# Performance work log

Hardware: AMD Instinct MI355X
Metric: run time of the kernel (lower is better)

Reference implementation:

```python
import jax, jax.numpy as jnp
import numpy as np

IN_FEATURES = 3
MAPPING_SIZE = 128
FF_SCALE = 10.0
HIDDEN = 512
HIDDEN_LAYERS = 5
OUT_FEATURES = 3
OMEGA0 = 30.0
TWO_PI = 2.0 * np.pi


def setup_inputs() -> dict:
    key = jax.random.key(0)
    ks = jax.random.split(key, 10)
    B, L = 1, 262144
    coords = jax.random.uniform(ks[0], (B, L, IN_FEATURES), jnp.float32, -1.0, 1.0)
    # Fourier feature projection (random Gaussian buffer, scale=10)
    B_ff = jax.random.normal(ks[1], (IN_FEATURES, MAPPING_SIZE), jnp.float32) * FF_SCALE
    ff_dim = 2 * MAPPING_SIZE  # 256
    # First sine layer: is_first=True -> U(-1/in, 1/in)
    W_first = jax.random.uniform(ks[2], (HIDDEN, ff_dim), jnp.float32, -1.0 / ff_dim, 1.0 / ff_dim)
    b_first = jax.random.uniform(ks[3], (HIDDEN,), jnp.float32, -1.0 / np.sqrt(ff_dim), 1.0 / np.sqrt(ff_dim))
    # Hidden sine layers: U(-sqrt(6/in)/omega0, +)
    wh = np.sqrt(6.0 / HIDDEN) / OMEGA0
    W_hidden = jax.random.uniform(ks[4], (HIDDEN_LAYERS, HIDDEN, HIDDEN), jnp.float32, -wh, wh)
    b_hidden = jax.random.uniform(ks[5], (HIDDEN_LAYERS, HIDDEN), jnp.float32, -1.0 / np.sqrt(HIDDEN), 1.0 / np.sqrt(HIDDEN))
    # Final linear: U(-sqrt(6/hidden)/omega0, +)
    W_out = jax.random.uniform(ks[6], (OUT_FEATURES, HIDDEN), jnp.float32, -wh, wh)
    b_out = jax.random.uniform(ks[7], (OUT_FEATURES,), jnp.float32, -1.0 / np.sqrt(HIDDEN), 1.0 / np.sqrt(HIDDEN))
    return {"coords": coords, "B_ff": B_ff, "W_first": W_first, "b_first": b_first,
            "W_hidden": W_hidden, "b_hidden": b_hidden, "W_out": W_out, "b_out": b_out}


def reference(coords, B_ff, W_first, b_first, W_hidden, b_hidden, W_out, b_out):
    # Fourier feature encoding: [B,L,3] -> [B,L,256]
    proj = TWO_PI * (coords @ B_ff)
    h = jnp.concatenate([jnp.sin(proj), jnp.cos(proj)], axis=-1)
    # First sine layer
    h = jnp.sin(OMEGA0 * (jnp.einsum('bli,oi->blo', h, W_first) + b_first))
    # Hidden sine layers (stacked weights, scanned)
    def step(h, wb):
        w, b = wb
        return jnp.sin(OMEGA0 * (jnp.einsum('bli,oi->blo', h, w) + b)), None
    h, _ = jax.lax.scan(step, h, (W_hidden, b_hidden))
    # Outermost linear
    return jnp.einsum('bli,oi->blo', h, W_out) + b_out
```

## Files before the change

### kernel.cpp

```cpp
#include <hip/hip_runtime.h>


#define L_TOTAL 262144
#define TOK 128
#define THREADS 512
#define C_SC 4.77464829275686f

typedef _Float16 f16x8 __attribute__((ext_vector_type(8)));
typedef _Float16 f16x4 __attribute__((ext_vector_type(4)));
typedef float    f32x4 __attribute__((ext_vector_type(4)));

#define N1 (512 * 256)
#define N2 (N1 + 5 * 512 * 512)
#define N3 (N2 + 16 * 512)
#define NBIAS 3072

__global__ void convert_weights(const float* __restrict__ Wf,
                                const float* __restrict__ Wh,
                                const float* __restrict__ Wo,
                                const float* __restrict__ bf,
                                const float* __restrict__ bh,
                                _Float16* __restrict__ o,
                                float* __restrict__ biasC) {
  int i = blockIdx.x * blockDim.x + threadIdx.x;
  if (i < N3) {
    float v;
    if (i < N1) {
      const int blk = i >> 9, w = i & 511;
      const int lane = w >> 3, e = w & 7;
      const int mt = blk >> 3, ks = blk & 7;
      const int row = mt * 16 + (lane & 15);
      const int col = ks * 32 + (lane >> 4) * 8 + e;
      v = Wf[row * 256 + col];
    } else if (i < N2) {
      int j = i - N1;
      const int l = j >> 18;
      j &= (1 << 18) - 1;
      const int blk = j >> 9, w = j & 511;
      const int lane = w >> 3, e = w & 7;
      const int mt = blk >> 4, ks = blk & 15;
      const int row = mt * 16 + (lane & 15);
      const int col = ks * 32 + (lane >> 4) * 8 + e;
      v = Wh[l * (512 * 512) + row * 512 + col];
    } else {
      const int r = (i - N2) >> 9, c = (i - N2) & 511;
      v = (r < 3) ? Wo[r * 512 + c] : 0.0f;
    }
    o[i] = (_Float16)v;
  } else if (i < N3 + NBIAS) {
    int j = i - N3;
    biasC[j] = (j < 512 ? bf[j] : bh[j - 512]) * C_SC;
  }
}

__device__ __forceinline__ int h_elem(int chunk, int token) {
  return (chunk * 128 + token) * 8;
}

template <int K>
__device__ __forceinline__ void sine_layer(const _Float16* __restrict__ W,
                                           const float* __restrict__ biasC,
                                           _Float16* hb, int lane, int lr,
                                           int lg, int m0) {
  constexpr int KS = K / 32;
  f32x4 acc[4][8];
#pragma unroll
  for (int mt = 0; mt < 4; ++mt)
#pragma unroll
    for (int nt = 0; nt < 8; ++nt)
      acc[mt][nt] = (f32x4){0.f, 0.f, 0.f, 0.f};

  const _Float16* wb[4];
#pragma unroll
  for (int mt = 0; mt < 4; ++mt)
    wb[mt] = &W[(((m0 >> 4) + mt) * KS) * 512 + lane * 8];

  f16x8 a[3][4], b[2][8];
#pragma unroll
  for (int mt = 0; mt < 4; ++mt) a[0][mt] = *(const f16x8*)(wb[mt]);
#pragma unroll
  for (int mt = 0; mt < 4; ++mt) a[1][mt] = *(const f16x8*)(wb[mt] + 512);
#pragma unroll
  for (int nt = 0; nt < 8; ++nt)
    b[0][nt] = *(const f16x8*)&hb[h_elem(lg, nt * 16 + lr)];

#pragma unroll
  for (int ks = 0; ks < KS; ++ks) {
    const int cur = ks & 1;
    const int ai = ks % 3;
    if (ks + 1 < KS) {
#pragma unroll
      for (int nt = 0; nt < 8; ++nt)
        b[cur ^ 1][nt] =
            *(const f16x8*)&hb[h_elem((ks + 1) * 4 + lg, nt * 16 + lr)];
    }
    if (ks + 2 < KS) {
#pragma unroll
      for (int mt = 0; mt < 4; ++mt)
        a[(ks + 2) % 3][mt] = *(const f16x8*)(wb[mt] + (ks + 2) * 512);
    }
#pragma unroll
    for (int mt = 0; mt < 4; ++mt)
#pragma unroll
      for (int nt = 0; nt < 8; ++nt)
        acc[mt][nt] = __builtin_amdgcn_mfma_f32_16x16x32_f16(
            a[ai][mt], b[cur][nt], acc[mt][nt], 0, 0, 0);
  }
  __syncthreads();

#pragma unroll
  for (int mt = 0; mt < 4; ++mt) {
    const int ob = m0 + mt * 16 + lg * 4;
    const f32x4 bb = *(const f32x4*)&biasC[ob];
    const int wbase = (ob >> 3) * 128 * 8 + (ob & 7);
#pragma unroll
    for (int nt = 0; nt < 8; ++nt) {
      f16x4 hv;
#pragma unroll
      for (int r = 0; r < 4; ++r) {
        float pre = fmaf(acc[mt][nt][r], C_SC, bb[r]);
        hv[r] = (_Float16)__builtin_amdgcn_sinf(__builtin_amdgcn_fractf(pre));
      }
      *(f16x4*)&hb[wbase + (nt * 16 + lr) * 8] = hv;
    }
  }
  __syncthreads();
}

__global__ __launch_bounds__(THREADS, 2) void siren_kernel(
    const float* __restrict__ coords, const float* __restrict__ bff,
    const float* __restrict__ biasC, const float* __restrict__ b_out,
    const _Float16* __restrict__ wf, const _Float16* __restrict__ wh,
    const _Float16* __restrict__ wo, float* __restrict__ out) {
  extern __shared__ _Float16 hb[];
  const int tid = threadIdx.x;
  const int t0 = blockIdx.x * TOK;

  {
    const int t = tid & 127;
    const int q = tid >> 7;
    const float c0 = coords[(t0 + t) * 3 + 0];
    const float c1 = coords[(t0 + t) * 3 + 1];
    const float c2 = coords[(t0 + t) * 3 + 2];
#pragma unroll
    for (int cb = 0; cb < 4; ++cb) {
      f16x8 sv, cv;
#pragma unroll
      for (int e = 0; e < 8; ++e) {
        const int j = q * 32 + cb * 8 + e;
        float r = fmaf(c0, bff[j], fmaf(c1, bff[128 + j], c2 * bff[256 + j]));
        float fr = __builtin_amdgcn_fractf(r);
        sv[e] = (_Float16)__builtin_amdgcn_sinf(fr);
        cv[e] = (_Float16)__builtin_amdgcn_cosf(fr);
      }
      *(f16x8*)&hb[h_elem(q * 4 + cb, t)] = sv;
      *(f16x8*)&hb[h_elem(16 + q * 4 + cb, t)] = cv;
    }
  }
  __syncthreads();

  const int lane = tid & 63;
  const int lr = lane & 15;
  const int lg = lane >> 4;
  const int m0 = (tid >> 6) * 64;

  sine_layer<256>(wf, biasC, hb, lane, lr, lg, m0);
#pragma unroll 1
  for (int l = 0; l < 5; ++l)
    sine_layer<512>(wh + l * (512 * 512), biasC + 512 + l * 512, hb, lane, lr,
                    lg, m0);

  {
    const int wave = tid >> 6;
    f32x4 acc = {0.f, 0.f, 0.f, 0.f};
#pragma unroll
    for (int ks = 0; ks < 16; ++ks) {
      f16x8 a = *(const f16x8*)&wo[lr * 512 + ks * 32 + lg * 8];
      f16x8 b = *(const f16x8*)&hb[h_elem(ks * 4 + lg, wave * 16 + lr)];
      acc = __builtin_amdgcn_mfma_f32_16x16x32_f16(a, b, acc, 0, 0, 0);
    }
    if (lg == 0) {
      const int t = t0 + wave * 16 + lr;
      out[t * 3 + 0] = acc[0] + b_out[0];
      out[t * 3 + 1] = acc[1] + b_out[1];
      out[t * 3 + 2] = acc[2] + b_out[2];
    }
  }
}

extern "C" void kernel_launch(void* const* d_in, const int* in_sizes, int n_in,
                              void* d_out, int out_size, void* d_ws,
                              size_t ws_size, hipStream_t stream) {
  const float* coords = (const float*)d_in[0];
  const float* bff    = (const float*)d_in[1];
  const float* Wf     = (const float*)d_in[2];
  const float* bf     = (const float*)d_in[3];
  const float* Wh     = (const float*)d_in[4];
  const float* bh     = (const float*)d_in[5];
  const float* Wo     = (const float*)d_in[6];
  const float* bo     = (const float*)d_in[7];
  float* out = (float*)d_out;

  _Float16* w16 = (_Float16*)d_ws;
  float* biasC = (float*)(w16 + N3);

  convert_weights<<<(N3 + NBIAS + 255) / 256, 256, 0, stream>>>(
      Wf, Wh, Wo, bf, bh, w16, biasC);

  const size_t lds_bytes = 64 * 128 * 8 * sizeof(_Float16);
  siren_kernel<<<L_TOTAL / TOK, THREADS, lds_bytes, stream>>>(
      coords, bff, biasC, bo, w16, w16 + N1, w16 + N2, out);
}
```

Measured before the change: 744.0 us.

## Split each layer into token halves and overlap sine epilogue with MFMA

Each sine layer is now computed as two half-token stages with separate accumulator sets. The sine/bias epilogue of the previous half is interleaved into the MFMA k-loop of the current half, so transcendental ALU work can hide behind matrix ops. Weight prefetch drops from a 3-deep to a 2-deep buffer, and the A tiles are reloaded for each half. This risks extra weight traffic and scheduling pressure from interleaving stores to LDS with the MFMA stream.

```diff
diff --git a/kernel.cpp b/kernel.cpp
--- a/kernel.cpp
+++ b/kernel.cpp
@@ -57,17 +57,39 @@
   return (chunk * 128 + token) * 8;
 }
 
-template <int K>
-__device__ __forceinline__ void sine_layer(const _Float16* __restrict__ W,
-                                           const float* __restrict__ biasC,
-                                           _Float16* hb, int lane, int lr,
-                                           int lg, int m0) {
+__device__ __forceinline__ void sine_epi(const float* __restrict__ biasEpi,
+                                         _Float16* hb, int lr, int lg, int m0,
+                                         int prevHalf, f32x4 (&accPrev)[4][4]) {
+#pragma unroll
+  for (int mt = 0; mt < 4; ++mt) {
+    const int ob = m0 + mt * 16 + lg * 4;
+    const f32x4 bb = *(const f32x4*)&biasEpi[ob];
+    const int wbase = (ob >> 3) * 128 * 8 + (ob & 7);
+#pragma unroll
+    for (int nt = 0; nt < 4; ++nt) {
+      f16x4 hv;
+#pragma unroll
+      for (int r = 0; r < 4; ++r) {
+        float pre = fmaf(accPrev[mt][nt][r], C_SC, bb[r]);
+        hv[r] = (_Float16)__builtin_amdgcn_sinf(__builtin_amdgcn_fractf(pre));
+      }
+      *(f16x4*)&hb[wbase + (prevHalf * 64 + nt * 16 + lr) * 8] = hv;
+    }
+  }
+}
+
+template <int K, bool EPI>
+__device__ __forceinline__ void sine_stage(
+    const _Float16* __restrict__ W, const float* __restrict__ biasEpi,
+    _Float16* hb, int lane, int lr, int lg, int m0, int half, int prevHalf,
+    f32x4 (&acc)[4][4], f32x4 (&accPrev)[4][4]) {
   constexpr int KS = K / 32;
-  f32x4 acc[4][8];
+  constexpr int EPO = 16 / KS;
+
 #pragma unroll
   for (int mt = 0; mt < 4; ++mt)
 #pragma unroll
-    for (int nt = 0; nt < 8; ++nt)
+    for (int nt = 0; nt < 4; ++nt)
       acc[mt][nt] = (f32x4){0.f, 0.f, 0.f, 0.f};
 
   const _Float16* wb[4];
@@ -75,56 +97,55 @@
   for (int mt = 0; mt < 4; ++mt)
     wb[mt] = &W[(((m0 >> 4) + mt) * KS) * 512 + lane * 8];
 
-  f16x8 a[3][4], b[2][8];
+  f32x4 bb[4];
+  if constexpr (EPI) {
+#pragma unroll
+    for (int mt = 0; mt < 4; ++mt)
+      bb[mt] = *(const f32x4*)&biasEpi[m0 + mt * 16 + lg * 4];
+  }
+
+  f16x8 a[2][4], b[2][4];
 #pragma unroll
   for (int mt = 0; mt < 4; ++mt) a[0][mt] = *(const f16x8*)(wb[mt]);
 #pragma unroll
-  for (int mt = 0; mt < 4; ++mt) a[1][mt] = *(const f16x8*)(wb[mt] + 512);
-#pragma unroll
-  for (int nt = 0; nt < 8; ++nt)
-    b[0][nt] = *(const f16x8*)&hb[h_elem(lg, nt * 16 + lr)];
+  for (int nt = 0; nt < 4; ++nt)
+    b[0][nt] = *(const f16x8*)&hb[h_elem(lg, half * 64 + nt * 16 + lr)];
 
 #pragma unroll
   for (int ks = 0; ks < KS; ++ks) {
     const int cur = ks & 1;
-    const int ai = ks % 3;
     if (ks + 1 < KS) {
 #pragma unroll
-      for (int nt = 0; nt < 8; ++nt)
-        b[cur ^ 1][nt] =
-            *(const f16x8*)&hb[h_elem((ks + 1) * 4 + lg, nt * 16 + lr)];
-    }
-    if (ks + 2 < KS) {
+      for (int nt = 0; nt < 4; ++nt)
+        b[cur ^ 1][nt] = *(const f16x8*)&hb[h_elem((ks + 1) * 4 + lg,
+                                                   half * 64 + nt * 16 + lr)];
 #pragma unroll
       for (int mt = 0; mt < 4; ++mt)
-        a[(ks + 2) % 3][mt] = *(const f16x8*)(wb[mt] + (ks + 2) * 512);
+        a[cur ^ 1][mt] = *(const f16x8*)(wb[mt] + (ks + 1) * 512);
+    }
+    if constexpr (EPI) {
+#pragma unroll
+      for (int u = 0; u < EPO; ++u) {
+        const int idx = ks * EPO + u;
+        const int mt = idx >> 2, nt = idx & 3;
+        const int ob = m0 + mt * 16 + lg * 4;
+        f16x4 hv;
+#pragma unroll
+        for (int r = 0; r < 4; ++r) {
+          float pre = fmaf(accPrev[mt][nt][r], C_SC, bb[mt][r]);
+          hv[r] = (_Float16)__builtin_amdgcn_sinf(__builtin_amdgcn_fractf(pre));
+        }
+        const int wbase = (ob >> 3) * 128 * 8 + (ob & 7);
+        *(f16x4*)&hb[wbase + (prevHalf * 64 + nt * 16 + lr) * 8] = hv;
+      }
     }
 #pragma unroll
     for (int mt = 0; mt < 4; ++mt)
 #pragma unroll
-      for (int nt = 0; nt < 8; ++nt)
+      for (int nt = 0; nt < 4; ++nt)
         acc[mt][nt] = __builtin_amdgcn_mfma_f32_16x16x32_f16(
-            a[ai][mt], b[cur][nt], acc[mt][nt], 0, 0, 0);
-  }
-  __syncthreads();
-
-#pragma unroll
-  for (int mt = 0; mt < 4; ++mt) {
-    const int ob = m0 + mt * 16 + lg * 4;
-    const f32x4 bb = *(const f32x4*)&biasC[ob];
-    const int wbase = (ob >> 3) * 128 * 8 + (ob & 7);
-#pragma unroll
-    for (int nt = 0; nt < 8; ++nt) {
-      f16x4 hv;
-#pragma unroll
-      for (int r = 0; r < 4; ++r) {
-        float pre = fmaf(acc[mt][nt][r], C_SC, bb[r]);
-        hv[r] = (_Float16)__builtin_amdgcn_sinf(__builtin_amdgcn_fractf(pre));
-      }
-      *(f16x4*)&hb[wbase + (nt * 16 + lr) * 8] = hv;
-    }
-  }
-  __syncthreads();
+            a[cur][mt], b[cur][nt], acc[mt][nt], 0, 0, 0);
+  }
 }
 
 __global__ __launch_bounds__(THREADS, 2) void siren_kernel(
@@ -164,11 +185,24 @@
   const int lg = lane >> 4;
   const int m0 = (tid >> 6) * 64;
 
-  sine_layer<256>(wf, biasC, hb, lane, lr, lg, m0);
+  f32x4 accA[4][4], accB[4][4];
+
+  sine_stage<256, false>(wf, nullptr, hb, lane, lr, lg, m0, 0, 0, accA, accB);
+  __syncthreads();
+  sine_stage<256, true>(wf, biasC, hb, lane, lr, lg, m0, 1, 0, accB, accA);
+  __syncthreads();
 #pragma unroll 1
-  for (int l = 0; l < 5; ++l)
-    sine_layer<512>(wh + l * (512 * 512), biasC + 512 + l * 512, hb, lane, lr,
-                    lg, m0);
+  for (int l = 0; l < 5; ++l) {
+    const _Float16* Wl = wh + l * (512 * 512);
+    const float* bPrev = (l == 0) ? biasC : biasC + 512 + (l - 1) * 512;
+    sine_stage<512, true>(Wl, bPrev, hb, lane, lr, lg, m0, 0, 1, accA, accB);
+    __syncthreads();
+    sine_stage<512, true>(Wl, biasC + 512 + l * 512, hb, lane, lr, lg, m0, 1, 0,
+                          accB, accA);
+    __syncthreads();
+  }
+  sine_epi(biasC + 512 + 4 * 512, hb, lr, lg, m0, 1, accB);
+  __syncthreads();
 
   {
     const int wave = tid >> 6;
```

Result: slower. 778.8 us (+4.7%).
